# Kernel optimization log

Measured on AMD Instinct MI355X. Metric: run time of the kernel, lower is better.

The kernel has to match this reference:

```python
import jax, jax.numpy as jnp
import numpy as np

N = 20000          # nodes
E = 320000         # edges (before self loops)
NG = 16            # graphs in batch
DIN = 256          # input_dim = heads*hidden
HID = 64           # hidden_dim
HEADS = 4
EPS = 1e-5         # LayerNorm eps
SLOPE = 0.2        # GATConv leaky_relu negative slope


def _ln(x, g, b):
    mu = jnp.mean(x, -1, keepdims=True)
    var = jnp.mean((x - mu) ** 2, -1, keepdims=True)
    return (x - mu) * jax.lax.rsqrt(var + EPS) * g + b


def _gat(x, src, dst, W, a_src, a_dst, bias, heads, out_dim, concat):
    # x: [N, F]; W: [F, heads*out_dim]; a_src/a_dst: [heads, out_dim]
    h = (x @ W).reshape(-1, heads, out_dim)              # [N, H, D]
    e_s = jnp.sum(h * a_src, -1)                         # [N, H]
    e_d = jnp.sum(h * a_dst, -1)                         # [N, H]
    e = jax.nn.leaky_relu(e_s[src] + e_d[dst], SLOPE)    # [E, H]
    # segment softmax over edges sharing the same target node
    m = jax.ops.segment_max(e, dst, num_segments=N)
    m = jnp.where(jnp.isfinite(m), m, 0.0)
    ex = jnp.exp(e - m[dst])
    s = jax.ops.segment_sum(ex, dst, num_segments=N)
    alpha = ex / (s[dst] + 1e-16)                        # [E, H]
    out = jax.ops.segment_sum(h[src] * alpha[:, :, None], dst, num_segments=N)
    out = out.reshape(-1, heads * out_dim) if concat else out.mean(1)
    return out + bias


def setup_inputs() -> dict:
    key = jax.random.key(0)
    ks = jax.random.split(key, 24)
    sc = 0.05
    inp = {
        "node_x": jax.random.normal(ks[0], (N, DIN), dtype=jnp.float32),
        "edge_index": jax.random.randint(ks[1], (2, E), 0, N, dtype=jnp.int64),
        "batch": jnp.sort(jax.random.randint(ks[2], (N,), 0, NG, dtype=jnp.int64)),
        # layer 1 (concat, heads=4)
        "W1": jax.random.normal(ks[3], (DIN, HEADS * HID), dtype=jnp.float32) * sc,
        "as1": jax.random.normal(ks[4], (HEADS, HID), dtype=jnp.float32) * sc,
        "ad1": jax.random.normal(ks[5], (HEADS, HID), dtype=jnp.float32) * sc,
        "b1": jnp.zeros((HEADS * HID,), dtype=jnp.float32),
        "g1": jnp.ones((HEADS * HID,), dtype=jnp.float32),
        "be1": jnp.zeros((HEADS * HID,), dtype=jnp.float32),
        # layer 2 (concat, heads=4)
        "W2": jax.random.normal(ks[6], (HEADS * HID, HEADS * HID), dtype=jnp.float32) * sc,
        "as2": jax.random.normal(ks[7], (HEADS, HID), dtype=jnp.float32) * sc,
        "ad2": jax.random.normal(ks[8], (HEADS, HID), dtype=jnp.float32) * sc,
        "b2": jnp.zeros((HEADS * HID,), dtype=jnp.float32),
        "g2": jnp.ones((HEADS * HID,), dtype=jnp.float32),
        "be2": jnp.zeros((HEADS * HID,), dtype=jnp.float32),
        # final (heads=1, averaged)
        "Wf": jax.random.normal(ks[9], (HEADS * HID, HID), dtype=jnp.float32) * sc,
        "asf": jax.random.normal(ks[10], (1, HID), dtype=jnp.float32) * sc,
        "adf": jax.random.normal(ks[11], (1, HID), dtype=jnp.float32) * sc,
        "bf": jnp.zeros((HID,), dtype=jnp.float32),
        "gf": jnp.ones((HID,), dtype=jnp.float32),
        "bef": jnp.zeros((HID,), dtype=jnp.float32),
    }
    return inp


def reference(node_x, edge_index, batch, W1, as1, ad1, b1, g1, be1,
              W2, as2, ad2, b2, g2, be2, Wf, asf, adf, bf, gf, bef):
    loops = jnp.arange(N, dtype=edge_index.dtype)
    src = jnp.concatenate([edge_index[0], loops])   # PyG add_self_loops=True
    dst = jnp.concatenate([edge_index[1], loops])

    x = node_x
    # layer 1 + LN + relu + residual (shapes match: DIN == HEADS*HID)
    r = x
    x = _gat(x, src, dst, W1, as1, ad1, b1, HEADS, HID, True)
    x = jax.nn.relu(_ln(x, g1, be1)) + r
    # layer 2
    r = x
    x = _gat(x, src, dst, W2, as2, ad2, b2, HEADS, HID, True)
    x = jax.nn.relu(_ln(x, g2, be2)) + r
    # final layer (heads=1, mean over heads), LN then relu
    x = _gat(x, src, dst, Wf, asf, adf, bf, 1, HID, False)
    x = jax.nn.relu(_ln(x, gf, bef))

    counts = jax.ops.segment_sum(jnp.ones((N,), x.dtype), batch, num_segments=NG)
    mean = jax.ops.segment_sum(x, batch, num_segments=NG) / jnp.clip(counts, 1.0)[:, None]
    mx = jax.ops.segment_max(x, batch, num_segments=NG)
    mx = jnp.where(jnp.isfinite(mx), mx, 0.0)
    pooled = jnp.concatenate([mean, mx], -1)
    return (x, pooled)
```

## Files before the change

### kernel.cpp

```cpp
#include <hip/hip_runtime.h>
#include <cstdint>
#include <cstddef>

#define NN 20000
#define EE 320000
#define TE (EE + NN)
#define NG 16
#define HEADS 4
#define LN_EPS 1e-5f
#define SLOPE 0.2f

typedef __attribute__((ext_vector_type(8))) short bfx8;
typedef __attribute__((ext_vector_type(8))) unsigned short u16x8;
typedef __attribute__((ext_vector_type(4))) float f32x4;
typedef __attribute__((ext_vector_type(8))) float f32x8;

__device__ __forceinline__ short f2bf(float f) {
    unsigned u = __float_as_uint(f);
    u += 0x7FFFu + ((u >> 16) & 1u);
    return (short)(u >> 16);
}
__device__ __forceinline__ float bf2f(unsigned short u) {
    return __uint_as_float(((unsigned)u) << 16);
}
__device__ __forceinline__ float lrelu(float e) {
    return (e >= 0.f) ? e : SLOPE * e;
}

__global__ void deg_kernel(const int* __restrict__ ei, int* __restrict__ counts) {
    int i = blockIdx.x * blockDim.x + threadIdx.x;
    if (i >= TE) return;
    int d = (i < EE) ? ei[EE + i] : (i - EE);
    atomicAdd(&counts[d], 1);
}

__global__ __launch_bounds__(256) void bsum_kernel(const int* __restrict__ cnt,
                                                   int* __restrict__ bsum) {
    int b = blockIdx.x;
    int i = b * 256 + threadIdx.x;
    int v = (i < NN) ? cnt[i] : 0;
    for (int s = 32; s > 0; s >>= 1) v += __shfl_down(v, s);
    __shared__ int ws4[4];
    int lane = threadIdx.x & 63, w = threadIdx.x >> 6;
    if (lane == 0) ws4[w] = v;
    __syncthreads();
    if (threadIdx.x == 0) bsum[b] = ws4[0] + ws4[1] + ws4[2] + ws4[3];
}

__global__ void bscan_kernel(const int* __restrict__ bsum, int* __restrict__ boff, int nb) {
    __shared__ int s[128];
    int t = threadIdx.x;
    int v = (t < nb) ? bsum[t] : 0;
    s[t] = v;
    __syncthreads();
    for (int st = 1; st < 128; st <<= 1) {
        int a = (t >= st) ? s[t - st] : 0;
        __syncthreads();
        s[t] += a;
        __syncthreads();
    }
    if (t < nb) boff[t] = s[t] - v;
}

__global__ __launch_bounds__(256) void offsets_kernel(const int* __restrict__ cnt,
                                                      const int* __restrict__ boff,
                                                      int* __restrict__ off,
                                                      int* __restrict__ cursor) {
    int b = blockIdx.x, t = threadIdx.x;
    int i = b * 256 + t;
    int v = (i < NN) ? cnt[i] : 0;
    int lane = t & 63, w = t >> 6;
    int x = v;
    for (int s = 1; s < 64; s <<= 1) {
        int u = __shfl_up(x, s);
        if (lane >= s) x += u;
    }
    __shared__ int wsum[4];
    if (lane == 63) wsum[w] = x;
    __syncthreads();
    int pre = 0;
    for (int k = 0; k < w; k++) pre += wsum[k];
    int excl = (x + pre - v) + boff[b];
    if (i < NN) { cursor[i] = excl; off[i] = excl; }
    if (i == NN - 1) off[NN] = excl + v;
}

__global__ void csr_fill_kernel(const int* __restrict__ ei, int* __restrict__ cursor,
                                int* __restrict__ csr_src) {
    int i = blockIdx.x * blockDim.x + threadIdx.x;
    if (i >= TE) return;
    int s, d;
    if (i < EE) { s = ei[i]; d = ei[EE + i]; }
    else        { s = i - EE; d = s; }
    int pos = atomicAdd(&cursor[d], 1);
    csr_src[pos] = s;
}

__global__ void gstart_kernel(const int* __restrict__ batch, int* __restrict__ gstart) {
    int g = threadIdx.x;
    if (g > NG) return;
    int lo = 0, hi = NN;
    while (lo < hi) {
        int mid = (lo + hi) >> 1;
        if (batch[mid] < g) lo = mid + 1; else hi = mid;
    }
    gstart[g] = lo;
}

__global__ void cvt_bf16_kernel(const float* __restrict__ in, unsigned short* __restrict__ out, int n4) {
    int i = blockIdx.x * blockDim.x + threadIdx.x;
    if (i >= n4) return;
    float4 v = ((const float4*)in)[i];
    ushort4 o;
    o.x = f2bf(v.x); o.y = f2bf(v.y); o.z = f2bf(v.z); o.w = f2bf(v.w);
    ((ushort4*)out)[i] = o;
}

__global__ __launch_bounds__(256) void transpose_cvt_kernel(const float* __restrict__ W,
                                                            short* __restrict__ WT,
                                                            int K, int Nc) {
    __shared__ float tile[32][33];
    int bx = blockIdx.x * 32;
    int by = blockIdx.y * 32;
    int tx = threadIdx.x & 31, ty = threadIdx.x >> 5;
    for (int r = ty; r < 32; r += 8)
        tile[r][tx] = W[(size_t)(by + r) * Nc + bx + tx];
    __syncthreads();
    for (int r = ty; r < 32; r += 8)
        WT[(size_t)(bx + r) * K + by + tx] = f2bf(tile[tx][r]);
}

#define GBM 64
#define GBN 64
#define GBK 64
__global__ __launch_bounds__(256) void gemm_attn_kernel(const short* __restrict__ A,
                                                        const short* __restrict__ BT,
                                                        unsigned short* __restrict__ Cb,
                                                        float* __restrict__ es,
                                                        float* __restrict__ ed,
                                                        const float* __restrict__ av_src,
                                                        const float* __restrict__ av_dst,
                                                        int M, int K, int Nc, int nheads) {
    __shared__ short Al[GBM * GBK];
    __shared__ short Bl[GBN * GBK];
    __shared__ float sps[64][2];
    __shared__ float spd[64][2];
    const int t = threadIdx.x;
    const int lane = t & 63, wid = t >> 6;
    const int wr = (wid >> 1) * 32, wc = (wid & 1) * 32;
    const int bm = blockIdx.x * GBM, bn = blockIdx.y * GBN;
    const int r0 = t >> 3, ch = t & 7;

    f32x4 acc[2][2] = {};

    for (int k0 = 0; k0 < K; k0 += GBK) {
#pragma unroll
        for (int p = 0; p < 2; p++) {
            int row = p * 32 + r0;
            int arow = bm + row; if (arow >= M) arow = M - 1;
            bfx8 av = *(const bfx8*)(A + (size_t)arow * K + k0 + ch * 8);
            bfx8 bv = *(const bfx8*)(BT + (size_t)(bn + row) * K + k0 + ch * 8);
            int wo = (row << 7) + (((ch ^ (row & 7))) << 4);
            *(bfx8*)((char*)Al + wo) = av;
            *(bfx8*)((char*)Bl + wo) = bv;
        }
        __syncthreads();
        bfx8 af[2][2], bfm[2][2];
#pragma unroll
        for (int m = 0; m < 2; m++)
#pragma unroll
            for (int kk = 0; kk < 2; kk++) {
                int rowa = wr + m * 16 + (lane & 15);
                int rowb = wc + m * 16 + (lane & 15);
                int c = kk * 4 + (lane >> 4);
                af[m][kk]  = *(const bfx8*)((const char*)Al + (rowa << 7) + (((c ^ (rowa & 7))) << 4));
                bfm[m][kk] = *(const bfx8*)((const char*)Bl + (rowb << 7) + (((c ^ (rowb & 7))) << 4));
            }
#pragma unroll
        for (int m = 0; m < 2; m++)
#pragma unroll
            for (int n = 0; n < 2; n++) {
                acc[m][n] = __builtin_amdgcn_mfma_f32_16x16x32_bf16(af[m][0], bfm[n][0], acc[m][n], 0, 0, 0);
                acc[m][n] = __builtin_amdgcn_mfma_f32_16x16x32_bf16(af[m][1], bfm[n][1], acc[m][n], 0, 0, 0);
            }
        __syncthreads();
    }

#pragma unroll
    for (int m = 0; m < 2; m++) {
        int row0 = bm + wr + m * 16 + ((lane >> 4) << 2);
#pragma unroll
        for (int n = 0; n < 2; n++) {
            int col = bn + wc + n * 16 + (lane & 15);
#pragma unroll
            for (int j = 0; j < 4; j++) {
                int row = row0 + j;
                if (row < M) Cb[(size_t)row * Nc + col] = (unsigned short)f2bf(acc[m][n][j]);
            }
        }
    }

    const int hd = bn >> 6;
    float asv[2], adv[2];
#pragma unroll
    for (int n = 0; n < 2; n++) {
        int c = wc + n * 16 + (lane & 15);
        asv[n] = av_src[hd * 64 + c];
        adv[n] = av_dst[hd * 64 + c];
    }
#pragma unroll
    for (int m = 0; m < 2; m++) {
#pragma unroll
        for (int j = 0; j < 4; j++) {
            float ps = acc[m][0][j] * asv[0] + acc[m][1][j] * asv[1];
            float pd = acc[m][0][j] * adv[0] + acc[m][1][j] * adv[1];
            ps += __shfl_xor(ps, 1); pd += __shfl_xor(pd, 1);
            ps += __shfl_xor(ps, 2); pd += __shfl_xor(pd, 2);
            ps += __shfl_xor(ps, 4); pd += __shfl_xor(pd, 4);
            ps += __shfl_xor(ps, 8); pd += __shfl_xor(pd, 8);
            if ((lane & 15) == 0) {
                int rl = wr + m * 16 + ((lane >> 4) << 2) + j;
                sps[rl][wid & 1] = ps;
                spd[rl][wid & 1] = pd;
            }
        }
    }
    __syncthreads();
    if (t < 64) {
        int row = bm + t;
        if (row < M) {
            es[(size_t)row * nheads + hd] = sps[t][0] + sps[t][1];
            ed[(size_t)row * nheads + hd] = spd[t][0] + spd[t][1];
        }
    }
}

__global__ __launch_bounds__(256) void gat_agg_ln_kernel(
    const unsigned short* __restrict__ hb,
    const float* __restrict__ es, const float* __restrict__ ed,
    const int* __restrict__ off, const int* __restrict__ csrs,
    const float* __restrict__ bias, const float* __restrict__ gamma, const float* __restrict__ beta,
    const float* __restrict__ residf, const unsigned short* __restrict__ residb,
    unsigned short* __restrict__ xbout) {
    const int wid = threadIdx.x >> 6, lane = threadIdx.x & 63;
    const int n = blockIdx.x * 4 + wid;
    const int half = lane >> 5, sl = lane & 31;
    const int hd = sl >> 3;
    const int d0 = sl * 8;
    const int j0 = off[n], j1 = off[n + 1];
    const float edn = ed[n * HEADS + hd];

    float acc[8] = {};
    float wsum = 0.f;
    int j = j0 + half;
    for (; j + 6 < j1; j += 8) {
        int s0 = csrs[j], s1 = csrs[j + 2], s2 = csrs[j + 4], s3 = csrs[j + 6];
        float w0 = __expf(lrelu(es[s0 * HEADS + hd] + edn));
        float w1 = __expf(lrelu(es[s1 * HEADS + hd] + edn));
        float w2 = __expf(lrelu(es[s2 * HEADS + hd] + edn));
        float w3 = __expf(lrelu(es[s3 * HEADS + hd] + edn));
        u16x8 r0 = *(const u16x8*)(hb + (size_t)s0 * 256 + d0);
        u16x8 r1 = *(const u16x8*)(hb + (size_t)s1 * 256 + d0);
        u16x8 r2 = *(const u16x8*)(hb + (size_t)s2 * 256 + d0);
        u16x8 r3 = *(const u16x8*)(hb + (size_t)s3 * 256 + d0);
        wsum += (w0 + w1) + (w2 + w3);
#pragma unroll
        for (int k = 0; k < 8; k++)
            acc[k] += w0 * bf2f(r0[k]) + w1 * bf2f(r1[k]) + w2 * bf2f(r2[k]) + w3 * bf2f(r3[k]);
    }
    for (; j < j1; j += 2) {
        int s = csrs[j];
        float wt = __expf(lrelu(es[s * HEADS + hd] + edn));
        u16x8 r = *(const u16x8*)(hb + (size_t)s * 256 + d0);
        wsum += wt;
#pragma unroll
        for (int k = 0; k < 8; k++) acc[k] += wt * bf2f(r[k]);
    }
    wsum += __shfl_xor(wsum, 32);
#pragma unroll
    for (int k = 0; k < 8; k++) acc[k] += __shfl_xor(acc[k], 32);

    float inv = 1.f / (wsum + 1e-16f);
    f32x8 bi = *(const f32x8*)(bias + d0);
    float v[8];
    float ls = 0.f, lq = 0.f;
#pragma unroll
    for (int k = 0; k < 8; k++) {
        v[k] = acc[k] * inv + bi[k];
        ls += v[k];
        lq += v[k] * v[k];
    }
    ls += __shfl_xor(ls, 1);  lq += __shfl_xor(lq, 1);
    ls += __shfl_xor(ls, 2);  lq += __shfl_xor(lq, 2);
    ls += __shfl_xor(ls, 4);  lq += __shfl_xor(lq, 4);
    ls += __shfl_xor(ls, 8);  lq += __shfl_xor(lq, 8);
    ls += __shfl_xor(ls, 16); lq += __shfl_xor(lq, 16);
    float mu = ls * (1.0f / 256.0f);
    float var = lq * (1.0f / 256.0f) - mu * mu;
    float rstd = rsqrtf(var + LN_EPS);
    f32x8 ga = *(const f32x8*)(gamma + d0);
    f32x8 be = *(const f32x8*)(beta + d0);
    f32x8 rs = {};
    if (half == 0) {
        if (residf) {
            rs = *(const f32x8*)(residf + (size_t)n * 256 + d0);
        } else {
            u16x8 rb = *(const u16x8*)(residb + (size_t)n * 256 + d0);
#pragma unroll
            for (int k = 0; k < 8; k++) rs[k] = bf2f(rb[k]);
        }
    }
    float y[8];
#pragma unroll
    for (int k = 0; k < 8; k++) {
        float yy = fmaxf((v[k] - mu) * rstd * ga[k] + be[k], 0.f) + rs[k];
        float tt = __shfl_xor(yy, 32);
        y[k] = half ? tt : yy;
    }
    if (half == 1) {
        u16x8 ob;
#pragma unroll
        for (int k = 0; k < 8; k++) ob[k] = (unsigned short)f2bf(y[k]);
        *(u16x8*)(xbout + (size_t)n * 256 + d0) = ob;
    }
}

__global__ __launch_bounds__(256) void gat_final_kernel(
    const unsigned short* __restrict__ hb,
    const float* __restrict__ es, const float* __restrict__ ed,
    const int* __restrict__ off, const int* __restrict__ csrs,
    const float* __restrict__ bias, const float* __restrict__ gamma, const float* __restrict__ beta,
    float* __restrict__ xout) {
    const int wid = threadIdx.x >> 6, lane = threadIdx.x & 63;
    const int n = blockIdx.x * 4 + wid;
    const int q = lane >> 4, sq = lane & 15;
    const int d0 = sq * 4;
    const int j0 = off[n], j1 = off[n + 1];
    const float edn = ed[n];

    float acc[4] = {};
    float wsum = 0.f;
    int j = j0 + q;
    for (; j + 4 < j1; j += 8) {
        int s0 = csrs[j], s1 = csrs[j + 4];
        float w0 = __expf(lrelu(es[s0] + edn));
        float w1 = __expf(lrelu(es[s1] + edn));
        ushort4 r0 = *(const ushort4*)(hb + (size_t)s0 * 64 + d0);
        ushort4 r1 = *(const ushort4*)(hb + (size_t)s1 * 64 + d0);
        wsum += w0 + w1;
        acc[0] += w0 * bf2f(r0.x) + w1 * bf2f(r1.x);
        acc[1] += w0 * bf2f(r0.y) + w1 * bf2f(r1.y);
        acc[2] += w0 * bf2f(r0.z) + w1 * bf2f(r1.z);
        acc[3] += w0 * bf2f(r0.w) + w1 * bf2f(r1.w);
    }
    for (; j < j1; j += 4) {
        int s = csrs[j];
        float wt = __expf(lrelu(es[s] + edn));
        ushort4 r = *(const ushort4*)(hb + (size_t)s * 64 + d0);
        wsum += wt;
        acc[0] += wt * bf2f(r.x);
        acc[1] += wt * bf2f(r.y);
        acc[2] += wt * bf2f(r.z);
        acc[3] += wt * bf2f(r.w);
    }
    wsum += __shfl_xor(wsum, 16);
    wsum += __shfl_xor(wsum, 32);
#pragma unroll
    for (int k = 0; k < 4; k++) {
        acc[k] += __shfl_xor(acc[k], 16);
        acc[k] += __shfl_xor(acc[k], 32);
    }
    float inv = 1.f / (wsum + 1e-16f);
    float4 bi = *(const float4*)(bias + d0);
    float v[4];
    float ls = 0.f, lq = 0.f;
    v[0] = acc[0] * inv + bi.x; v[1] = acc[1] * inv + bi.y;
    v[2] = acc[2] * inv + bi.z; v[3] = acc[3] * inv + bi.w;
#pragma unroll
    for (int k = 0; k < 4; k++) { ls += v[k]; lq += v[k] * v[k]; }
    ls += __shfl_xor(ls, 1); lq += __shfl_xor(lq, 1);
    ls += __shfl_xor(ls, 2); lq += __shfl_xor(lq, 2);
    ls += __shfl_xor(ls, 4); lq += __shfl_xor(lq, 4);
    ls += __shfl_xor(ls, 8); lq += __shfl_xor(lq, 8);
    float mu = ls * (1.0f / 64.0f);
    float var = lq * (1.0f / 64.0f) - mu * mu;
    float rstd = rsqrtf(var + LN_EPS);
    if (q == 0) {
        float4 ga = *(const float4*)(gamma + d0);
        float4 be = *(const float4*)(beta + d0);
        float4 o;
        o.x = fmaxf((v[0] - mu) * rstd * ga.x + be.x, 0.f);
        o.y = fmaxf((v[1] - mu) * rstd * ga.y + be.y, 0.f);
        o.z = fmaxf((v[2] - mu) * rstd * ga.z + be.z, 0.f);
        o.w = fmaxf((v[3] - mu) * rstd * ga.w + be.w, 0.f);
        *(float4*)(xout + (size_t)n * 64 + d0) = o;
    }
}

__global__ __launch_bounds__(256) void pool_partial_kernel(
    const float* __restrict__ x, const int* __restrict__ gstart,
    float* __restrict__ gsum, unsigned* __restrict__ gmax) {
    int g = blockIdx.x, sp = blockIdx.y;
    int r0 = gstart[g], r1 = gstart[g + 1];
    int t = threadIdx.x, d = t & 63, rg = t >> 6;
    float sum = 0.f, mx = 0.f;
    for (int r = r0 + sp * 4 + rg; r < r1; r += 32) {
        float v = x[(size_t)r * 64 + d];
        sum += v;
        mx = fmaxf(mx, v);
    }
    __shared__ float S[256], M[256];
    S[t] = sum; M[t] = mx;
    __syncthreads();
    if (t < 64) {
        float s4 = S[t] + S[t + 64] + S[t + 128] + S[t + 192];
        float m4 = fmaxf(fmaxf(M[t], M[t + 64]), fmaxf(M[t + 128], M[t + 192]));
        atomicAdd(&gsum[g * 64 + t], s4);
        atomicMax(&gmax[g * 64 + t], __float_as_uint(m4));
    }
}

__global__ void pool_final_kernel(const float* __restrict__ gsum,
                                  const unsigned* __restrict__ gmax,
                                  const int* __restrict__ gstart,
                                  float* __restrict__ pout) {
    int g = blockIdx.x, d = threadIdx.x;
    float c = fmaxf((float)(gstart[g + 1] - gstart[g]), 1.0f);
    pout[g * 128 + d] = gsum[g * 64 + d] / c;
    pout[g * 128 + 64 + d] = __uint_as_float(gmax[g * 64 + d]);
}

extern "C" void kernel_launch(void* const* d_in, const int* in_sizes, int n_in,
                              void* d_out, int out_size, void* d_ws, size_t ws_size,
                              hipStream_t stream) {
    const float* node_x = (const float*)d_in[0];
    const int*   ei     = (const int*)d_in[1];
    const int*   batch  = (const int*)d_in[2];
    const float* W1  = (const float*)d_in[3];
    const float* as1 = (const float*)d_in[4];
    const float* ad1 = (const float*)d_in[5];
    const float* b1  = (const float*)d_in[6];
    const float* g1  = (const float*)d_in[7];
    const float* be1 = (const float*)d_in[8];
    const float* W2  = (const float*)d_in[9];
    const float* as2 = (const float*)d_in[10];
    const float* ad2 = (const float*)d_in[11];
    const float* b2  = (const float*)d_in[12];
    const float* g2  = (const float*)d_in[13];
    const float* be2 = (const float*)d_in[14];
    const float* Wf  = (const float*)d_in[15];
    const float* asf = (const float*)d_in[16];
    const float* adf = (const float*)d_in[17];
    const float* bf  = (const float*)d_in[18];
    const float* gf  = (const float*)d_in[19];
    const float* bef = (const float*)d_in[20];
    float* out = (float*)d_out;

    char* w = (char*)d_ws;
    auto alloc = [&](size_t bytes) -> void* {
        void* p = (void*)w;
        w += (bytes + 255) & ~(size_t)255;
        return p;
    };
    unsigned short* hb   = (unsigned short*)alloc((size_t)NN * 256 * 2);
    unsigned short* xbA  = (unsigned short*)alloc((size_t)NN * 256 * 2);
    unsigned short* xbB  = (unsigned short*)alloc((size_t)NN * 256 * 2);
    short*          wt   = (short*)alloc((size_t)256 * 256 * 2);
    float*          es   = (float*)alloc((size_t)NN * HEADS * 4);
    float*          ed   = (float*)alloc((size_t)NN * HEADS * 4);
    int*      counts = (int*)alloc((size_t)NN * 4);
    int*      off    = (int*)alloc((size_t)(NN + 1) * 4);
    int*      cursor = (int*)alloc((size_t)NN * 4);
    int*      csrs   = (int*)alloc((size_t)TE * 4);
    int*      bsum   = (int*)alloc((size_t)128 * 4);
    int*      boff   = (int*)alloc((size_t)128 * 4);
    float*    gsum   = (float*)alloc((size_t)NG * 64 * 4);
    unsigned* gmax   = (unsigned*)alloc((size_t)NG * 64 * 4);
    int*      gstart = (int*)alloc((size_t)(NG + 1) * 4);

    hipMemsetAsync(counts, 0, (size_t)NN * 4, stream);
    hipMemsetAsync(gsum, 0, (size_t)NG * 64 * 4, stream);
    hipMemsetAsync(gmax, 0, (size_t)NG * 64 * 4, stream);

    const int NB = (NN + 255) / 256;
    const int EB = (TE + 255) / 256;

    deg_kernel<<<EB, 256, 0, stream>>>(ei, counts);
    bsum_kernel<<<NB, 256, 0, stream>>>(counts, bsum);
    bscan_kernel<<<1, 128, 0, stream>>>(bsum, boff, NB);
    offsets_kernel<<<NB, 256, 0, stream>>>(counts, boff, off, cursor);
    csr_fill_kernel<<<EB, 256, 0, stream>>>(ei, cursor, csrs);
    gstart_kernel<<<1, 32, 0, stream>>>(batch, gstart);

    const int n4 = NN * 256 / 4;
    dim3 tg256(8, 8), tg64(2, 8);
    dim3 gg256((NN + GBM - 1) / GBM, 256 / GBN);
    dim3 gg64((NN + GBM - 1) / GBM, 1);

    cvt_bf16_kernel<<<(n4 + 255) / 256, 256, 0, stream>>>(node_x, xbA, n4);
    transpose_cvt_kernel<<<tg256, 256, 0, stream>>>(W1, wt, 256, 256);
    gemm_attn_kernel<<<gg256, 256, 0, stream>>>((const short*)xbA, wt, hb, es, ed, as1, ad1, NN, 256, 256, HEADS);
    gat_agg_ln_kernel<<<NN / 4, 256, 0, stream>>>(hb, es, ed, off, csrs, b1, g1, be1, node_x, nullptr, xbB);
    transpose_cvt_kernel<<<tg256, 256, 0, stream>>>(W2, wt, 256, 256);
    gemm_attn_kernel<<<gg256, 256, 0, stream>>>((const short*)xbB, wt, hb, es, ed, as2, ad2, NN, 256, 256, HEADS);
    gat_agg_ln_kernel<<<NN / 4, 256, 0, stream>>>(hb, es, ed, off, csrs, b2, g2, be2, nullptr, xbB, xbA);
    transpose_cvt_kernel<<<tg64, 256, 0, stream>>>(Wf, wt, 256, 64);
    gemm_attn_kernel<<<gg64, 256, 0, stream>>>((const short*)xbA, wt, hb, es, ed, asf, adf, NN, 256, 64, 1);
    gat_final_kernel<<<NN / 4, 256, 0, stream>>>(hb, es, ed, off, csrs, bf, gf, bef, out);
    pool_partial_kernel<<<dim3(NG, 8), 256, 0, stream>>>(out, gstart, gsum, gmax);
    pool_final_kernel<<<NG, 64, 0, stream>>>(gsum, gmax, gstart, out + (size_t)NN * 64);
}
```

Measured before the change: 283.1 us.

## Fuse input bf16 conversion into GEMM and batch weight transposes

Result: faster. 277.4 us, median of 2 (-2.0%).

```diff
diff --git a/kernel.cpp b/kernel.cpp
--- a/kernel.cpp
+++ b/kernel.cpp
@@ -107,33 +107,30 @@
     gstart[g] = lo;
 }
 
-__global__ void cvt_bf16_kernel(const float* __restrict__ in, unsigned short* __restrict__ out, int n4) {
-    int i = blockIdx.x * blockDim.x + threadIdx.x;
-    if (i >= n4) return;
-    float4 v = ((const float4*)in)[i];
-    ushort4 o;
-    o.x = f2bf(v.x); o.y = f2bf(v.y); o.z = f2bf(v.z); o.w = f2bf(v.w);
-    ((ushort4*)out)[i] = o;
-}
-
-__global__ __launch_bounds__(256) void transpose_cvt_kernel(const float* __restrict__ W,
-                                                            short* __restrict__ WT,
-                                                            int K, int Nc) {
+__global__ __launch_bounds__(256) void transpose_all_kernel(
+    const float* __restrict__ W1, const float* __restrict__ W2, const float* __restrict__ Wf,
+    short* __restrict__ wt1, short* __restrict__ wt2, short* __restrict__ wtf) {
     __shared__ float tile[32][33];
+    int z = blockIdx.z;
+    const float* W = (z == 0) ? W1 : (z == 1) ? W2 : Wf;
+    short* WT = (z == 0) ? wt1 : (z == 1) ? wt2 : wtf;
+    int Nc = (z == 2) ? 64 : 256;
     int bx = blockIdx.x * 32;
     int by = blockIdx.y * 32;
+    if (bx >= Nc) return;
     int tx = threadIdx.x & 31, ty = threadIdx.x >> 5;
     for (int r = ty; r < 32; r += 8)
         tile[r][tx] = W[(size_t)(by + r) * Nc + bx + tx];
     __syncthreads();
     for (int r = ty; r < 32; r += 8)
-        WT[(size_t)(bx + r) * K + by + tx] = f2bf(tile[tx][r]);
+        WT[(size_t)(bx + r) * 256 + by + tx] = f2bf(tile[tx][r]);
 }
 
 #define GBM 64
 #define GBN 64
 #define GBK 64
-__global__ __launch_bounds__(256) void gemm_attn_kernel(const short* __restrict__ A,
+template<bool AF32>
+__global__ __launch_bounds__(256) void gemm_attn_kernel(const void* __restrict__ Ap,
                                                         const short* __restrict__ BT,
                                                         unsigned short* __restrict__ Cb,
                                                         float* __restrict__ es,
@@ -148,7 +145,7 @@
     const int t = threadIdx.x;
     const int lane = t & 63, wid = t >> 6;
     const int wr = (wid >> 1) * 32, wc = (wid & 1) * 32;
-    const int bm = blockIdx.x * GBM, bn = blockIdx.y * GBN;
+    const int bm = blockIdx.y * GBM, bn = blockIdx.x * GBN;
     const int r0 = t >> 3, ch = t & 7;
 
     f32x4 acc[2][2] = {};
@@ -158,7 +155,18 @@
         for (int p = 0; p < 2; p++) {
             int row = p * 32 + r0;
             int arow = bm + row; if (arow >= M) arow = M - 1;
-            bfx8 av = *(const bfx8*)(A + (size_t)arow * K + k0 + ch * 8);
+            bfx8 av;
+            if constexpr (AF32) {
+                const float* A = (const float*)Ap;
+                const float* src = A + (size_t)arow * K + k0 + ch * 8;
+                float4 f0 = *(const float4*)(src);
+                float4 f1 = *(const float4*)(src + 4);
+                av[0] = f2bf(f0.x); av[1] = f2bf(f0.y); av[2] = f2bf(f0.z); av[3] = f2bf(f0.w);
+                av[4] = f2bf(f1.x); av[5] = f2bf(f1.y); av[6] = f2bf(f1.z); av[7] = f2bf(f1.w);
+            } else {
+                const short* A = (const short*)Ap;
+                av = *(const bfx8*)(A + (size_t)arow * K + k0 + ch * 8);
+            }
             bfx8 bv = *(const bfx8*)(BT + (size_t)(bn + row) * K + k0 + ch * 8);
             int wo = (row << 7) + (((ch ^ (row & 7))) << 4);
             *(bfx8*)((char*)Al + wo) = av;
@@ -465,7 +473,9 @@
     unsigned short* hb   = (unsigned short*)alloc((size_t)NN * 256 * 2);
     unsigned short* xbA  = (unsigned short*)alloc((size_t)NN * 256 * 2);
     unsigned short* xbB  = (unsigned short*)alloc((size_t)NN * 256 * 2);
-    short*          wt   = (short*)alloc((size_t)256 * 256 * 2);
+    short*          wt1  = (short*)alloc((size_t)256 * 256 * 2);
+    short*          wt2  = (short*)alloc((size_t)256 * 256 * 2);
+    short*          wtf  = (short*)alloc((size_t)64 * 256 * 2);
     float*          es   = (float*)alloc((size_t)NN * HEADS * 4);
     float*          ed   = (float*)alloc((size_t)NN * HEADS * 4);
     int*      counts = (int*)alloc((size_t)NN * 4);
@@ -492,20 +502,16 @@
     csr_fill_kernel<<<EB, 256, 0, stream>>>(ei, cursor, csrs);
     gstart_kernel<<<1, 32, 0, stream>>>(batch, gstart);
 
-    const int n4 = NN * 256 / 4;
-    dim3 tg256(8, 8), tg64(2, 8);
-    dim3 gg256((NN + GBM - 1) / GBM, 256 / GBN);
-    dim3 gg64((NN + GBM - 1) / GBM, 1);
-
-    cvt_bf16_kernel<<<(n4 + 255) / 256, 256, 0, stream>>>(node_x, xbA, n4);
-    transpose_cvt_kernel<<<tg256, 256, 0, stream>>>(W1, wt, 256, 256);
-    gemm_attn_kernel<<<gg256, 256, 0, stream>>>((const short*)xbA, wt, hb, es, ed, as1, ad1, NN, 256, 256, HEADS);
+    transpose_all_kernel<<<dim3(8, 8, 3), 256, 0, stream>>>(W1, W2, Wf, wt1, wt2, wtf);
+
+    dim3 gg256(4, (NN + GBM - 1) / GBM);
+    dim3 gg64(1, (NN + GBM - 1) / GBM);
+
+    gemm_attn_kernel<true><<<gg256, 256, 0, stream>>>(node_x, wt1, hb, es, ed, as1, ad1, NN, 256, 256, HEADS);
     gat_agg_ln_kernel<<<NN / 4, 256, 0, stream>>>(hb, es, ed, off, csrs, b1, g1, be1, node_x, nullptr, xbB);
-    transpose_cvt_kernel<<<tg256, 256, 0, stream>>>(W2, wt, 256, 256);
-    gemm_attn_kernel<<<gg256, 256, 0, stream>>>((const short*)xbB, wt, hb, es, ed, as2, ad2, NN, 256, 256, HEADS);
+    gemm_attn_kernel<false><<<gg256, 256, 0, stream>>>(xbB, wt2, hb, es, ed, as2, ad2, NN, 256, 256, HEADS);
     gat_agg_ln_kernel<<<NN / 4, 256, 0, stream>>>(hb, es, ed, off, csrs, b2, g2, be2, nullptr, xbB, xbA);
-    transpose_cvt_kernel<<<tg64, 256, 0, stream>>>(Wf, wt, 256, 64);
-    gemm_attn_kernel<<<gg64, 256, 0, stream>>>((const short*)xbA, wt, hb, es, ed, asf, adf, NN, 256, 64, 1);
+    gemm_attn_kernel<false><<<gg64, 256, 0, stream>>>(xbA, wtf, hb, es, ed, asf, adf, NN, 256, 64, 1);
     gat_final_kernel<<<NN / 4, 256, 0, stream>>>(hb, es, ed, off, csrs, bf, gf, bef, out);
     pool_partial_kernel<<<dim3(NG, 8), 256, 0, stream>>>(out, gstart, gsum, gmax);
     pool_final_kernel<<<NG, 64, 0, stream>>>(gsum, gmax, gstart, out + (size_t)NN * 64);
```
